# Kernel tuning notes

Hardware: AMD Instinct MI355X
Metric: run time of the kernel (lower is better)

Reference implementation:

```python
import jax, jax.numpy as jnp
import numpy as np

EPS = 1e-8
NUM_ITER = 3
NUM_SLOTS = 8
NUM_HEADS = 4


def _ln(x, w, b):
    m = x.mean(-1, keepdims=True)
    v = x.var(-1, keepdims=True)
    return (x - m) / jnp.sqrt(v + 1e-5) * w + b


def setup_inputs() -> dict:
    key = jax.random.key(0)
    B, T, N, D, S, H = 16, 12, 1024, 256, 128, 256
    K = NUM_SLOTS
    ks = jax.random.split(key, 32)
    w = lambda i, shape: (0.02 * jax.random.normal(ks[i], shape)).astype(jnp.float32)
    f32 = jnp.float32
    return {
        'inputs': jax.random.normal(ks[0], (B, T, N, D), f32),
        'slots_noise': jax.random.normal(ks[1], (B, K, S), f32),
        'slot_mu': w(2, (1, 1, S)),
        'slot_log_sigma': w(3, (1, 1, S)),
        'ln_in_w': jnp.ones((D,), f32), 'ln_in_b': jnp.zeros((D,), f32),
        'ln_slots_w': jnp.ones((S,), f32), 'ln_slots_b': jnp.zeros((S,), f32),
        'ln_mlp_w': jnp.ones((S,), f32), 'ln_mlp_b': jnp.zeros((S,), f32),
        'Wq': w(4, (S, S)), 'Wk': w(5, (D, S)), 'Wv': w(6, (D, S)),
        'gru_Wih': w(7, (3 * S, S)), 'gru_Whh': w(8, (3 * S, S)),
        'gru_bih': jnp.zeros((3 * S,), f32), 'gru_bhh': jnp.zeros((3 * S,), f32),
        'mlp_W1': w(9, (S, H)), 'mlp_b1': jnp.zeros((H,), f32),
        'mlp_W2': w(10, (H, S)), 'mlp_b2': jnp.zeros((S,), f32),
        'p_ln1_w': jnp.ones((S,), f32), 'p_ln1_b': jnp.zeros((S,), f32),
        'p_Wq': w(11, (S, S)), 'p_Wk': w(12, (S, S)), 'p_Wv': w(13, (S, S)), 'p_Wo': w(14, (S, S)),
        'p_ln2_w': jnp.ones((S,), f32), 'p_ln2_b': jnp.zeros((S,), f32),
        'p_ffn_W1': w(15, (S, 4 * S)), 'p_ffn_b1': jnp.zeros((4 * S,), f32),
        'p_ffn_W2': w(16, (4 * S, S)), 'p_ffn_b2': jnp.zeros((S,), f32),
        'p_lnf_w': jnp.ones((S,), f32), 'p_lnf_b': jnp.zeros((S,), f32),
    }


def reference(inputs, slots_noise, slot_mu, slot_log_sigma,
              ln_in_w, ln_in_b, ln_slots_w, ln_slots_b, ln_mlp_w, ln_mlp_b,
              Wq, Wk, Wv, gru_Wih, gru_Whh, gru_bih, gru_bhh,
              mlp_W1, mlp_b1, mlp_W2, mlp_b2,
              p_ln1_w, p_ln1_b, p_Wq, p_Wk, p_Wv, p_Wo,
              p_ln2_w, p_ln2_b, p_ffn_W1, p_ffn_b1, p_ffn_W2, p_ffn_b2,
              p_lnf_w, p_lnf_b):
    B, T, N, D = inputs.shape
    S = slot_mu.shape[-1]
    K = NUM_SLOTS

    slots0 = slot_mu + jnp.exp(slot_log_sigma) * slots_noise  # (B,K,S)
    x = _ln(inputs, ln_in_w, ln_in_b)
    k = (x @ Wk) * (S ** -0.5)  # (B,T,N,S), pre-scaled keys
    v = x @ Wv                  # (B,T,N,S)

    def gru(u, h):  # torch GRUCell semantics; u,h: (B*K,S)
        gi = u @ gru_Wih.T + gru_bih
        gh = h @ gru_Whh.T + gru_bhh
        i_r, i_z, i_n = jnp.split(gi, 3, -1)
        h_r, h_z, h_n = jnp.split(gh, 3, -1)
        r = jax.nn.sigmoid(i_r + h_r)
        z = jax.nn.sigmoid(i_z + h_z)
        n = jnp.tanh(i_n + r * h_n)
        return (1.0 - z) * n + z * h

    def mha(y):  # (B,K,S) self-attention, pre-LN block style
        dh = S // NUM_HEADS
        split = lambda t: t.reshape(B, K, NUM_HEADS, dh).transpose(0, 2, 1, 3)
        q = split(y @ p_Wq) * (dh ** -0.5)
        kk = split(y @ p_Wk)
        vv = split(y @ p_Wv)
        a = jax.nn.softmax(jnp.einsum('bhqd,bhkd->bhqk', q, kk), -1)
        o = jnp.einsum('bhqk,bhkd->bhqd', a, vv).transpose(0, 2, 1, 3).reshape(B, K, S)
        return o @ p_Wo

    def predictor(s):
        s = s + mha(_ln(s, p_ln1_w, p_ln1_b))
        h = _ln(s, p_ln2_w, p_ln2_b)
        s = s + (jax.nn.relu(h @ p_ffn_W1 + p_ffn_b1) @ p_ffn_W2 + p_ffn_b2)
        return _ln(s, p_lnf_w, p_lnf_b)

    def step(slots, kv_t):
        k_t, v_t = kv_t  # (B,N,S) each
        attn_vis = None
        for i in range(NUM_ITER):
            slots_prev = slots
            q = _ln(slots, ln_slots_w, ln_slots_b) @ Wq          # (B,K,S)
            logits = jnp.einsum('bns,bks->bnk', k_t, q)           # (B,N,K)
            attn_vis = jax.nn.softmax(logits, -1)                 # over slots
            attn = attn_vis + EPS
            attn = attn / attn.sum(1, keepdims=True)              # normalize over inputs
            updates = jnp.einsum('bnk,bns->bks', attn, v_t)       # (B,K,S)
            slots = gru(updates.reshape(-1, S), slots_prev.reshape(-1, S)).reshape(B, K, S)
            if i < NUM_ITER - 1:
                h = _ln(slots, ln_mlp_w, ln_mlp_b)
                slots = slots + (jax.nn.relu(h @ mlp_W1 + mlp_b1) @ mlp_W2 + mlp_b2)
        return predictor(slots), (slots, attn_vis)

    kT = jnp.swapaxes(k, 0, 1)  # (T,B,N,S)
    vT = jnp.swapaxes(v, 0, 1)
    _, (slots_seq, attn_seq) = jax.lax.scan(step, slots0, (kT, vT))
    slots_collect = jnp.swapaxes(slots_seq, 0, 1)  # (B,T,K,S)
    attns_collect = jnp.swapaxes(attn_seq, 0, 1)   # (B,T,N,K)
    return slots_collect, attns_collect
```

## Files before the change

### kernel.cpp

```cpp
#include <hip/hip_runtime.h>
#include <hip/hip_bf16.h>

typedef _Float16 half8 __attribute__((ext_vector_type(8)));
typedef float floatx4 __attribute__((ext_vector_type(4)));

#define MFMA_F16(a, b, c) __builtin_amdgcn_mfma_f32_16x16x32_f16((a), (b), (c), 0, 0, 0)

struct PrepJobs {
  const float* src[11];
  _Float16* dst[11];
  int In[11], Out[11], elems[11], doT[11];
  float scale[11];
};

__global__ void prep_all_kernel(PrepJobs J) {
  int j = blockIdx.y;
  int idx = blockIdx.x * 256 + threadIdx.x;
  if (idx >= J.elems[j]) return;
  float v;
  if (J.doT[j]) { int o = idx / J.In[j], i = idx - o * J.In[j]; v = J.src[j][i * J.Out[j] + o]; }
  else          { v = J.src[j][idx]; }
  J.dst[j][idx] = (_Float16)(v * J.scale[j]);
}

__global__ void prep_wtilde_kernel(const float* __restrict__ Wk, const float* __restrict__ Wq,
                                   _Float16* __restrict__ WT, float scale) {
  int idx = blockIdx.x * 256 + threadIdx.x;
  int s = idx >> 8, i = idx & 255;
  const float* wk = Wk + (size_t)i * 128;
  const float* wq = Wq + (size_t)s * 128;
  float acc = 0.f;
  #pragma unroll 4
  for (int o = 0; o < 128; o++) acc += wk[o] * wq[o];
  WT[idx] = (_Float16)(acc * scale);
}

__global__ void init_ctr_kernel(int* __restrict__ ctr) {
  ctr[threadIdx.x] = 0;
}

__global__ __launch_bounds__(256) void gemm_kv_kernel(
    const float* __restrict__ x, const float* __restrict__ lnw_g,
    const float* __restrict__ lnb_g, const _Float16* __restrict__ WT,
    _Float16* __restrict__ kout, _Float16* __restrict__ vTout) {
  __shared__ union {
    struct { _Float16 A[128][72]; _Float16 B[128][72]; } s;
    _Float16 C[128][136];
  } u;
  __shared__ float s_mean[128], s_rstd[128], s_red[256][2], s_lnw[256], s_lnb[256];

  const int tid = threadIdx.x;
  const int bx = blockIdx.x, y = blockIdx.y;
  const size_t r0 = (size_t)bx * 128;
  const int w = tid >> 6, lane = tid & 63, quad = lane >> 4, l15 = lane & 15;

  s_lnw[tid] = lnw_g[tid];
  s_lnb[tid] = lnb_g[tid];
  {
    int row = tid >> 1, half = tid & 1;
    const float* p = x + (r0 + row) * 256 + half * 128;
    float s = 0.f, sq = 0.f;
    for (int i = 0; i < 32; i++) {
      float4 d = ((const float4*)p)[i];
      s += d.x + d.y + d.z + d.w;
      sq += d.x * d.x + d.y * d.y + d.z * d.z + d.w * d.w;
    }
    s_red[tid][0] = s; s_red[tid][1] = sq;
  }
  __syncthreads();
  if (tid < 128) {
    float s  = s_red[2 * tid][0] + s_red[2 * tid + 1][0];
    float sq = s_red[2 * tid][1] + s_red[2 * tid + 1][1];
    float m = s * (1.f / 256.f);
    float v = sq * (1.f / 256.f) - m * m;
    s_mean[tid] = m; s_rstd[tid] = rsqrtf(v + 1e-5f);
  }

  floatx4 acc[2][8];
  for (int rt = 0; rt < 2; rt++)
    for (int ct = 0; ct < 8; ct++) acc[rt][ct] = (floatx4){0.f, 0.f, 0.f, 0.f};

  for (int c = 0; c < 4; c++) {
    __syncthreads();
    for (int i = 0; i < 4; i++) {
      int g = tid + 256 * i;
      int row = g >> 3, c8 = g & 7;
      int col0 = c * 64 + c8 * 8;
      const float* p = x + (r0 + row) * 256 + col0;
      float4 d0 = ((const float4*)p)[0];
      float4 d1 = ((const float4*)p)[1];
      float f[8] = {d0.x, d0.y, d0.z, d0.w, d1.x, d1.y, d1.z, d1.w};
      float m = s_mean[row], rs = s_rstd[row];
      half8 hv;
      #pragma unroll
      for (int j = 0; j < 8; j++)
        hv[j] = (_Float16)((f[j] - m) * rs * s_lnw[col0 + j] + s_lnb[col0 + j]);
      *(half8*)&u.s.A[row][c8 * 8] = hv;
      *(half8*)&u.s.B[row][c8 * 8] = *(const half8*)(WT + (size_t)(y * 128 + row) * 256 + col0);
    }
    __syncthreads();
    #pragma unroll
    for (int ks = 0; ks < 2; ks++) {
      half8 af[2];
      af[0] = *(const half8*)&u.s.A[(2 * w) * 16 + l15][ks * 32 + quad * 8];
      af[1] = *(const half8*)&u.s.A[(2 * w + 1) * 16 + l15][ks * 32 + quad * 8];
      #pragma unroll
      for (int ct = 0; ct < 8; ct++) {
        half8 bf = *(const half8*)&u.s.B[ct * 16 + l15][ks * 32 + quad * 8];
        acc[0][ct] = MFMA_F16(af[0], bf, acc[0][ct]);
        acc[1][ct] = MFMA_F16(af[1], bf, acc[1][ct]);
      }
    }
  }

  const size_t bt = (size_t)(bx >> 3);
  const int n0loc = (bx & 7) * 128;
  if (y == 0) {
    for (int rt = 0; rt < 2; rt++)
      for (int ct = 0; ct < 8; ct++)
        #pragma unroll
        for (int r = 0; r < 4; r++) {
          size_t row = r0 + (2 * w + rt) * 16 + quad * 4 + r;
          kout[row * 128 + ct * 16 + l15] = (_Float16)acc[rt][ct][r];
        }
  } else {
    __syncthreads();
    for (int rt = 0; rt < 2; rt++)
      for (int ct = 0; ct < 8; ct++)
        #pragma unroll
        for (int r = 0; r < 4; r++)
          u.C[(2 * w + rt) * 16 + quad * 4 + r][ct * 16 + l15] = (_Float16)acc[rt][ct][r];
    __syncthreads();
    int s = tid >> 1, hf = tid & 1;
    for (int j = 0; j < 8; j++) {
      int nb = hf * 64 + j * 8;
      half8 tmp;
      #pragma unroll
      for (int e = 0; e < 8; e++) tmp[e] = u.C[nb + e][s];
      *(half8*)(vTout + (bt * 128 + s) * 1024 + n0loc + nb) = tmp;
    }
  }
}

struct P2Args {
  const _Float16 *kbuf, *vT;
  const _Float16 *Wih, *Whh, *W1T, *W2T;
  const _Float16 *pQT, *pKT, *pVT, *pOT, *pF1T, *pF2T;
  const float *noise, *mu, *lsig;
  const float *lnsw, *lnsb, *lnmw, *lnmb;
  const float *bih, *bhh, *mb1, *mb2;
  const float *pl1w, *pl1b, *pl2w, *pl2b, *fb1, *fb2, *plfw, *plfb;
  float *out_slots, *out_attn;
  float *upd_p;
  float *col_p;
  float *vs_p;
  int   *ctr;
};

struct SH {
  _Float16 k_lds[128][136];
  _Float16 v_lds[128][136];
  float slots[8][128];
  _Float16 a16[16][136];
  _Float16 h16[16][136];
  float gi[8][384];
  float gh[8][384];
  union {
    struct { _Float16 qT[16][136]; _Float16 attnT[16][136]; } sa;
    struct { _Float16 m16[16][264]; } mlp;
    struct { float qh[8][128]; float kh[8][128]; float vh[8][128]; float sc[4][8][8]; } mha;
    struct { _Float16 f16[16][520]; } ffn;
  } u;
  float colsum[8];
  float vsum[128];
  float bih[384], bhh[384], mb1[256], mb2[128], fb1[512], fb2[128];
  float lnsw[128], lnsb[128], lnmw[128], lnmb[128];
  float pl1w[128], pl1b[128], pl2w[128], pl2b[128], plfw[128], plfb[128];
};

__device__ __forceinline__ void group_barrier(int* ctr, int target) {
  __syncthreads();
  if (threadIdx.x == 0) {
    __hip_atomic_fetch_add(ctr, 1, __ATOMIC_ACQ_REL, __HIP_MEMORY_SCOPE_AGENT);
    while (__hip_atomic_load(ctr, __ATOMIC_ACQUIRE, __HIP_MEMORY_SCOPE_AGENT) < target)
      __builtin_amdgcn_s_sleep(1);
  }
  __syncthreads();
}

__device__ __forceinline__ void ln_to_a16(SH* sh, const float (*src)[128],
                                          const float* wv, const float* bv,
                                          int w, int lane) {
  if (w < 8) {
    float x0 = src[w][lane], x1 = src[w][lane + 64];
    float s = x0 + x1, sq = x0 * x0 + x1 * x1;
    #pragma unroll
    for (int m = 1; m < 64; m <<= 1) { s += __shfl_xor(s, m); sq += __shfl_xor(sq, m); }
    float mn = s * 0.0078125f;
    float vr = sq * 0.0078125f - mn * mn;
    float rs = rsqrtf(vr + 1e-5f);
    sh->a16[w][lane]      = (_Float16)((x0 - mn) * rs * wv[lane]      + bv[lane]);
    sh->a16[w][lane + 64] = (_Float16)((x1 - mn) * rs * wv[lane + 64] + bv[lane + 64]);
  } else {
    sh->a16[w][lane] = (_Float16)0.f;
    sh->a16[w][lane + 64] = (_Float16)0.f;
  }
}

__global__ __launch_bounds__(1024, 4) void slot_attn_kernel(P2Args P) {
  __shared__ SH sh;
  const int tid = threadIdx.x;
  const int w = tid >> 6, lane = tid & 63, quad = lane >> 4, l15 = lane & 15;
  const int b = blockIdx.x & 15;
  const int g = blockIdx.x >> 4;
  const int n0 = g * 128;
  int* ctrb = P.ctr + b * 64;
  int bar_phase = 0;

  for (int i = tid; i < 384; i += 1024) { sh.bih[i] = P.bih[i]; sh.bhh[i] = P.bhh[i]; }
  for (int i = tid; i < 256; i += 1024) sh.mb1[i] = P.mb1[i];
  for (int i = tid; i < 512; i += 1024) sh.fb1[i] = P.fb1[i];
  if (tid < 128) {
    sh.mb2[tid]  = P.mb2[tid];  sh.fb2[tid]  = P.fb2[tid];
    sh.lnsw[tid] = P.lnsw[tid]; sh.lnsb[tid] = P.lnsb[tid];
    sh.lnmw[tid] = P.lnmw[tid]; sh.lnmb[tid] = P.lnmb[tid];
    sh.pl1w[tid] = P.pl1w[tid]; sh.pl1b[tid] = P.pl1b[tid];
    sh.pl2w[tid] = P.pl2w[tid]; sh.pl2b[tid] = P.pl2b[tid];
    sh.plfw[tid] = P.plfw[tid]; sh.plfb[tid] = P.plfb[tid];
  }
  {
    int kk = tid >> 7, s = tid & 127;
    sh.slots[kk][s] = P.mu[s] + expf(P.lsig[s]) * P.noise[(b * 8 + kk) * 128 + s];
  }
  __syncthreads();

  for (int t = 0; t < 12; t++) {
    const _Float16* kt = P.kbuf + ((size_t)(b * 12 + t)) * 1024 * 128 + (size_t)n0 * 128;
    const _Float16* vt = P.vT   + ((size_t)(b * 12 + t)) * 128 * 1024 + n0;
    {
      int r = tid >> 4, c8 = (tid & 15) * 8;
      #pragma unroll
      for (int p = 0; p < 2; p++) {
        int row = p * 64 + r;
        *(half8*)&sh.k_lds[row][c8] = *(const half8*)(kt + (size_t)row * 128 + c8);
        *(half8*)&sh.v_lds[row][c8] = *(const half8*)(vt + (size_t)row * 1024 + c8);
      }
    }
    if (tid < 128) sh.vsum[tid] = 0.f;
    __syncthreads();
    {
      int s = tid >> 3, j = tid & 7;
      float a = 0.f;
      #pragma unroll
      for (int e = 0; e < 16; e++) a += (float)sh.v_lds[s][j * 16 + e];
      atomicAdd(&sh.vsum[s], a);
    }
    __syncthreads();
    if (tid < 128)
      __hip_atomic_store(&P.vs_p[(b * 8 + g) * 128 + tid], sh.vsum[tid],
                         __ATOMIC_RELAXED, __HIP_MEMORY_SCOPE_AGENT);

    for (int it = 0; it < 3; it++) {
      const int par = (t * 3 + it) & 1;
      float* updg = P.upd_p + ((size_t)(par * 16 + b) * 8 + g) * 1024;
      float* colg = P.col_p + ((size_t)(par * 16 + b) * 8 + g) * 64;
      if (w < 8) {
        float x0 = sh.slots[w][lane], x1 = sh.slots[w][lane + 64];
        sh.h16[w][lane] = (_Float16)x0; sh.h16[w][lane + 64] = (_Float16)x1;
        float s = x0 + x1, sq = x0 * x0 + x1 * x1;
        #pragma unroll
        for (int m = 1; m < 64; m <<= 1) { s += __shfl_xor(s, m); sq += __shfl_xor(sq, m); }
        float mn = s * 0.0078125f;
        float vr = sq * 0.0078125f - mn * mn;
        float rs = rsqrtf(vr + 1e-5f);
        sh.a16[w][lane]      = (_Float16)((x0 - mn) * rs * sh.lnsw[lane]      + sh.lnsb[lane]);
        sh.a16[w][lane + 64] = (_Float16)((x1 - mn) * rs * sh.lnsw[lane + 64] + sh.lnsb[lane + 64]);
      } else {
        sh.h16[w][lane] = (_Float16)0.f; sh.h16[w][lane + 64] = (_Float16)0.f;
        sh.a16[w][lane] = (_Float16)0.f; sh.a16[w][lane + 64] = (_Float16)0.f;
      }
      if (tid < 8) sh.colsum[tid] = 0.f;
      __syncthreads();
      if (w < 8) {
        int nloc0 = w * 16;
        floatx4 acc = (floatx4){0.f, 0.f, 0.f, 0.f};
        const _Float16* ar = &sh.k_lds[nloc0 + l15][quad * 8];
        const _Float16* br = &sh.a16[l15][quad * 8];
        #pragma unroll
        for (int ks = 0; ks < 4; ks++)
          acc = MFMA_F16(*(const half8*)(ar + ks * 32), *(const half8*)(br + ks * 32), acc);
        float cs = 0.f;
        #pragma unroll
        for (int r = 0; r < 4; r++) {
          float v = (l15 < 8) ? acc[r] : -3.0e38f;
          float mx = v;
          mx = fmaxf(mx, __shfl_xor(mx, 1, 16));
          mx = fmaxf(mx, __shfl_xor(mx, 2, 16));
          mx = fmaxf(mx, __shfl_xor(mx, 4, 16));
          mx = fmaxf(mx, __shfl_xor(mx, 8, 16));
          float pv = (l15 < 8) ? expf(v - mx) : 0.f;
          float ss = pv;
          ss += __shfl_xor(ss, 1, 16); ss += __shfl_xor(ss, 2, 16);
          ss += __shfl_xor(ss, 4, 16); ss += __shfl_xor(ss, 8, 16);
          float pn = pv / ss;
          cs += pn;
          int nloc = nloc0 + quad * 4 + r;
          sh.u.sa.attnT[l15][nloc] = (_Float16)pn;
          if (it == 2 && l15 < 8)
            P.out_attn[((size_t)(b * 12 + t) * 1024 + n0 + nloc) * 8 + l15] = pn;
        }
        cs += __shfl_xor(cs, 16); cs += __shfl_xor(cs, 32);
        if (lane < 8) atomicAdd(&sh.colsum[lane], cs);
      } else {
        const int idx8 = w - 8;
        const _Float16* ar = &sh.h16[l15][quad * 8];
        #pragma unroll
        for (int tt = 0; tt < 2; tt++) {
          int ct = idx8 + tt * 8;
          const _Float16* Bg = P.Whh + (size_t)(ct * 16 + l15) * 128 + quad * 8;
          floatx4 acc = (floatx4){0.f, 0.f, 0.f, 0.f};
          #pragma unroll
          for (int ks = 0; ks < 4; ks++)
            acc = MFMA_F16(*(const half8*)(ar + ks * 32), *(const half8*)(Bg + ks * 32), acc);
          int col = ct * 16 + l15;
          #pragma unroll
          for (int r = 0; r < 4; r++) {
            int slot = quad * 4 + r;
            if (slot < 8) sh.gh[slot][col] = acc[r] + sh.bhh[col];
          }
        }
      }
      __syncthreads();
      if (w < 8) {
        floatx4 acc = (floatx4){0.f, 0.f, 0.f, 0.f};
        const _Float16* ar = &sh.u.sa.attnT[l15][quad * 8];
        const _Float16* br = &sh.v_lds[w * 16 + l15][quad * 8];
        #pragma unroll
        for (int ks = 0; ks < 4; ks++)
          acc = MFMA_F16(*(const half8*)(ar + ks * 32), *(const half8*)(br + ks * 32), acc);
        int scol = w * 16 + l15;
        #pragma unroll
        for (int r = 0; r < 4; r++) {
          int slot = quad * 4 + r;
          if (slot < 8)
            __hip_atomic_store(&updg[slot * 128 + scol], acc[r],
                               __ATOMIC_RELAXED, __HIP_MEMORY_SCOPE_AGENT);
        }
      } else {
        const int idx8 = w - 8;
        int ct = idx8 + 16;
        const _Float16* ar = &sh.h16[l15][quad * 8];
        const _Float16* Bg = P.Whh + (size_t)(ct * 16 + l15) * 128 + quad * 8;
        floatx4 acc = (floatx4){0.f, 0.f, 0.f, 0.f};
        #pragma unroll
        for (int ks = 0; ks < 4; ks++)
          acc = MFMA_F16(*(const half8*)(ar + ks * 32), *(const half8*)(Bg + ks * 32), acc);
        int col = ct * 16 + l15;
        #pragma unroll
        for (int r = 0; r < 4; r++) {
          int slot = quad * 4 + r;
          if (slot < 8) sh.gh[slot][col] = acc[r] + sh.bhh[col];
        }
      }
      if (tid < 8)
        __hip_atomic_store(&colg[tid], sh.colsum[tid],
                           __ATOMIC_RELAXED, __HIP_MEMORY_SCOPE_AGENT);
      bar_phase++;
      group_barrier(ctrb, 8 * bar_phase);
      {
        int slot = tid >> 7, scol = tid & 127;
        const float* up = P.upd_p + (size_t)(par * 16 + b) * 8 * 1024 + slot * 128 + scol;
        float sum = 0.f;
        #pragma unroll
        for (int gg = 0; gg < 8; gg++)
          sum += __hip_atomic_load((float*)(up + gg * 1024),
                                   __ATOMIC_RELAXED, __HIP_MEMORY_SCOPE_AGENT);
        const float* cp = P.col_p + (size_t)(par * 16 + b) * 8 * 64 + slot;
        float csum = 0.f;
        #pragma unroll
        for (int gg = 0; gg < 8; gg++)
          csum += __hip_atomic_load((float*)(cp + gg * 64),
                                    __ATOMIC_RELAXED, __HIP_MEMORY_SCOPE_AGENT);
        float vsv;
        if (it == 0) {
          const float* vp = P.vs_p + b * 8 * 128 + scol;
          float vtot = 0.f;
          #pragma unroll
          for (int gg = 0; gg < 8; gg++)
            vtot += __hip_atomic_load((float*)(vp + gg * 128),
                                      __ATOMIC_RELAXED, __HIP_MEMORY_SCOPE_AGENT);
          if (slot == 0) sh.vsum[scol] = vtot;
          vsv = vtot;
        } else {
          vsv = sh.vsum[scol];
        }
        float upd = (sum + 1e-8f * vsv) / (csum + 1024.f * 1e-8f);
        sh.a16[slot][scol] = (_Float16)upd;
      }
      __syncthreads();
      {
        const _Float16* ar = &sh.a16[l15][quad * 8];
        const _Float16* Bg = P.Wih + (size_t)(w * 16 + l15) * 128 + quad * 8;
        floatx4 acc = (floatx4){0.f, 0.f, 0.f, 0.f};
        #pragma unroll
        for (int ks = 0; ks < 4; ks++)
          acc = MFMA_F16(*(const half8*)(ar + ks * 32), *(const half8*)(Bg + ks * 32), acc);
        int col = w * 16 + l15;
        #pragma unroll
        for (int r = 0; r < 4; r++) {
          int slot = quad * 4 + r;
          if (slot < 8) sh.gi[slot][col] = acc[r] + sh.bih[col];
        }
        if (w < 8) {
          int col2 = (16 + w) * 16 + l15;
          const _Float16* Bg2 = P.Wih + (size_t)((16 + w) * 16 + l15) * 128 + quad * 8;
          floatx4 acc2 = (floatx4){0.f, 0.f, 0.f, 0.f};
          #pragma unroll
          for (int ks = 0; ks < 4; ks++)
            acc2 = MFMA_F16(*(const half8*)(ar + ks * 32), *(const half8*)(Bg2 + ks * 32), acc2);
          #pragma unroll
          for (int r = 0; r < 4; r++) {
            int slot = quad * 4 + r;
            if (slot < 8) sh.gi[slot][col2] = acc2[r] + sh.bih[col2];
          }
        }
      }
      __syncthreads();
      if (w < 8) {
        float h0 = sh.slots[w][lane], h1 = sh.slots[w][lane + 64];
        float r0 = 1.f / (1.f + expf(-(sh.gi[w][lane]       + sh.gh[w][lane])));
        float z0 = 1.f / (1.f + expf(-(sh.gi[w][128 + lane] + sh.gh[w][128 + lane])));
        float n0v = tanhf(sh.gi[w][256 + lane] + r0 * sh.gh[w][256 + lane]);
        float x0 = (1.f - z0) * n0v + z0 * h0;
        int l64 = lane + 64;
        float r1 = 1.f / (1.f + expf(-(sh.gi[w][l64]       + sh.gh[w][l64])));
        float z1 = 1.f / (1.f + expf(-(sh.gi[w][128 + l64] + sh.gh[w][128 + l64])));
        float n1v = tanhf(sh.gi[w][256 + l64] + r1 * sh.gh[w][256 + l64]);
        float x1 = (1.f - z1) * n1v + z1 * h1;
        sh.slots[w][lane] = x0; sh.slots[w][lane + 64] = x1;
        if (it == 2 && g == 0) {
          P.out_slots[((size_t)(b * 12 + t) * 8 + w) * 128 + lane]      = x0;
          P.out_slots[((size_t)(b * 12 + t) * 8 + w) * 128 + lane + 64] = x1;
        }
        const float* wv = (it < 2) ? sh.lnmw : sh.pl1w;
        const float* bv = (it < 2) ? sh.lnmb : sh.pl1b;
        float s = x0 + x1, sq = x0 * x0 + x1 * x1;
        #pragma unroll
        for (int m = 1; m < 64; m <<= 1) { s += __shfl_xor(s, m); sq += __shfl_xor(sq, m); }
        float mn = s * 0.0078125f;
        float vr = sq * 0.0078125f - mn * mn;
        float rs = rsqrtf(vr + 1e-5f);
        sh.a16[w][lane]      = (_Float16)((x0 - mn) * rs * wv[lane]      + bv[lane]);
        sh.a16[w][lane + 64] = (_Float16)((x1 - mn) * rs * wv[lane + 64] + bv[lane + 64]);
      }
      __syncthreads();
      if (it < 2) {
        {
          floatx4 acc = (floatx4){0.f, 0.f, 0.f, 0.f};
          const _Float16* ar = &sh.a16[l15][quad * 8];
          const _Float16* br = P.W1T + (size_t)(w * 16 + l15) * 128 + quad * 8;
          #pragma unroll
          for (int ks = 0; ks < 4; ks++)
            acc = MFMA_F16(*(const half8*)(ar + ks * 32), *(const half8*)(br + ks * 32), acc);
          int col = w * 16 + l15;
          #pragma unroll
          for (int r = 0; r < 4; r++) {
            int slot = quad * 4 + r;
            if (slot < 8) sh.u.mlp.m16[slot][col] = (_Float16)fmaxf(acc[r] + sh.mb1[col], 0.f);
            else          sh.u.mlp.m16[slot][col] = (_Float16)0.f;
          }
        }
        __syncthreads();
        if (w < 8) {
          floatx4 acc = (floatx4){0.f, 0.f, 0.f, 0.f};
          const _Float16* ar = &sh.u.mlp.m16[l15][quad * 8];
          const _Float16* br = P.W2T + (size_t)(w * 16 + l15) * 256 + quad * 8;
          #pragma unroll
          for (int ks = 0; ks < 8; ks++)
            acc = MFMA_F16(*(const half8*)(ar + ks * 32), *(const half8*)(br + ks * 32), acc);
          int col = w * 16 + l15;
          #pragma unroll
          for (int r = 0; r < 4; r++) {
            int slot = quad * 4 + r;
            if (slot < 8) sh.slots[slot][col] += acc[r] + sh.mb2[col];
          }
        }
        __syncthreads();
      }
    }

    {
      const _Float16* ar = &sh.a16[l15][quad * 8];
      int gg = w >> 3, ct = w & 7, col = ct * 16 + l15;
      const _Float16* Bg = (gg == 0 ? P.pQT : P.pKT) + (size_t)(ct * 16 + l15) * 128 + quad * 8;
      floatx4 acc = (floatx4){0.f, 0.f, 0.f, 0.f};
      #pragma unroll
      for (int ks = 0; ks < 4; ks++)
        acc = MFMA_F16(*(const half8*)(ar + ks * 32), *(const half8*)(Bg + ks * 32), acc);
      float scale = (gg == 0) ? 0.17677669529663687f : 1.f;
      float* dst = (gg == 0) ? &sh.u.mha.qh[0][0] : &sh.u.mha.kh[0][0];
      #pragma unroll
      for (int r = 0; r < 4; r++) {
        int slot = quad * 4 + r;
        if (slot < 8) dst[slot * 128 + col] = acc[r] * scale;
      }
      if (w < 8) {
        const _Float16* Bg2 = P.pVT + (size_t)(w * 16 + l15) * 128 + quad * 8;
        floatx4 a2 = (floatx4){0.f, 0.f, 0.f, 0.f};
        #pragma unroll
        for (int ks = 0; ks < 4; ks++)
          a2 = MFMA_F16(*(const half8*)(ar + ks * 32), *(const half8*)(Bg2 + ks * 32), a2);
        int colv = w * 16 + l15;
        #pragma unroll
        for (int r = 0; r < 4; r++) {
          int slot = quad * 4 + r;
          if (slot < 8) sh.u.mha.vh[slot][colv] = a2[r];
        }
      }
    }
    __syncthreads();
    if (w < 4) {
      int h = w, a = lane >> 3, b2 = lane & 7;
      const float* qr = &sh.u.mha.qh[a][h * 32];
      const float* kr = &sh.u.mha.kh[b2][h * 32];
      float s = 0.f;
      #pragma unroll
      for (int d = 0; d < 32; d++) s += qr[d] * kr[d];
      float mx = s;
      mx = fmaxf(mx, __shfl_xor(mx, 1, 8));
      mx = fmaxf(mx, __shfl_xor(mx, 2, 8));
      mx = fmaxf(mx, __shfl_xor(mx, 4, 8));
      float e = expf(s - mx);
      float ssum = e;
      ssum += __shfl_xor(ssum, 1, 8); ssum += __shfl_xor(ssum, 2, 8); ssum += __shfl_xor(ssum, 4, 8);
      float p = e / ssum;
      float o0 = 0.f, o1 = 0.f, o2 = 0.f, o3 = 0.f;
      int d0 = h * 32 + b2 * 4;
      #pragma unroll
      for (int j = 0; j < 8; j++) {
        float pj = __shfl(p, (a << 3) + j);
        const float* vr = &sh.u.mha.vh[j][d0];
        o0 += pj * vr[0]; o1 += pj * vr[1]; o2 += pj * vr[2]; o3 += pj * vr[3];
      }
      sh.a16[a][d0]     = (_Float16)o0;
      sh.a16[a][d0 + 1] = (_Float16)o1;
      sh.a16[a][d0 + 2] = (_Float16)o2;
      sh.a16[a][d0 + 3] = (_Float16)o3;
    }
    __syncthreads();
    if (w < 8) {
      floatx4 acc = (floatx4){0.f, 0.f, 0.f, 0.f};
      const _Float16* ar = &sh.a16[l15][quad * 8];
      const _Float16* br = P.pOT + (size_t)(w * 16 + l15) * 128 + quad * 8;
      #pragma unroll
      for (int ks = 0; ks < 4; ks++)
        acc = MFMA_F16(*(const half8*)(ar + ks * 32), *(const half8*)(br + ks * 32), acc);
      int col = w * 16 + l15;
      #pragma unroll
      for (int r = 0; r < 4; r++) {
        int slot = quad * 4 + r;
        if (slot < 8) sh.slots[slot][col] += acc[r];
      }
    }
    __syncthreads();
    ln_to_a16(&sh, sh.slots, sh.pl2w, sh.pl2b, w, lane);
    __syncthreads();
    for (int ct = w; ct < 32; ct += 16) {
      floatx4 acc = (floatx4){0.f, 0.f, 0.f, 0.f};
      const _Float16* ar = &sh.a16[l15][quad * 8];
      const _Float16* br = P.pF1T + (size_t)(ct * 16 + l15) * 128 + quad * 8;
      #pragma unroll
      for (int ks = 0; ks < 4; ks++)
        acc = MFMA_F16(*(const half8*)(ar + ks * 32), *(const half8*)(br + ks * 32), acc);
      int col = ct * 16 + l15;
      #pragma unroll
      for (int r = 0; r < 4; r++) {
        int slot = quad * 4 + r;
        if (slot < 8) sh.u.ffn.f16[slot][col] = (_Float16)fmaxf(acc[r] + sh.fb1[col], 0.f);
        else          sh.u.ffn.f16[slot][col] = (_Float16)0.f;
      }
    }
    __syncthreads();
    if (w < 8) {
      floatx4 acc = (floatx4){0.f, 0.f, 0.f, 0.f};
      const _Float16* ar = &sh.u.ffn.f16[l15][quad * 8];
      const _Float16* br = P.pF2T + (size_t)(w * 16 + l15) * 512 + quad * 8;
      #pragma unroll 4
      for (int ks = 0; ks < 16; ks++)
        acc = MFMA_F16(*(const half8*)(ar + ks * 32), *(const half8*)(br + ks * 32), acc);
      int col = w * 16 + l15;
      #pragma unroll
      for (int r = 0; r < 4; r++) {
        int slot = quad * 4 + r;
        if (slot < 8) sh.slots[slot][col] += acc[r] + sh.fb2[col];
      }
    }
    __syncthreads();
    if (w < 8) {
      float x0 = sh.slots[w][lane], x1 = sh.slots[w][lane + 64];
      float s = x0 + x1, sq = x0 * x0 + x1 * x1;
      #pragma unroll
      for (int m = 1; m < 64; m <<= 1) { s += __shfl_xor(s, m); sq += __shfl_xor(sq, m); }
      float mn = s * 0.0078125f;
      float vr = sq * 0.0078125f - mn * mn;
      float rs = rsqrtf(vr + 1e-5f);
      sh.slots[w][lane]      = (x0 - mn) * rs * sh.plfw[lane]      + sh.plfb[lane];
      sh.slots[w][lane + 64] = (x1 - mn) * rs * sh.plfw[lane + 64] + sh.plfb[lane + 64];
    }
    __syncthreads();
  }
}

extern "C" void kernel_launch(void* const* d_in, const int* in_sizes, int n_in,
                              void* d_out, int out_size, void* d_ws, size_t ws_size,
                              hipStream_t stream) {
  const float* inp   = (const float*)d_in[0];
  const float* noise = (const float*)d_in[1];
  const float* mu    = (const float*)d_in[2];
  const float* lsig  = (const float*)d_in[3];
  const float* lniw  = (const float*)d_in[4];
  const float* lnib  = (const float*)d_in[5];
  const float* lnsw  = (const float*)d_in[6];
  const float* lnsb  = (const float*)d_in[7];
  const float* lnmw  = (const float*)d_in[8];
  const float* lnmb  = (const float*)d_in[9];
  const float* Wq    = (const float*)d_in[10];
  const float* Wk    = (const float*)d_in[11];
  const float* Wv    = (const float*)d_in[12];
  const float* gWih  = (const float*)d_in[13];
  const float* gWhh  = (const float*)d_in[14];
  const float* gbih  = (const float*)d_in[15];
  const float* gbhh  = (const float*)d_in[16];
  const float* mW1   = (const float*)d_in[17];
  const float* mb1   = (const float*)d_in[18];
  const float* mW2   = (const float*)d_in[19];
  const float* mb2   = (const float*)d_in[20];
  const float* pl1w  = (const float*)d_in[21];
  const float* pl1b  = (const float*)d_in[22];
  const float* pWq   = (const float*)d_in[23];
  const float* pWk   = (const float*)d_in[24];
  const float* pWv   = (const float*)d_in[25];
  const float* pWo   = (const float*)d_in[26];
  const float* pl2w  = (const float*)d_in[27];
  const float* pl2b  = (const float*)d_in[28];
  const float* pf1   = (const float*)d_in[29];
  const float* pfb1  = (const float*)d_in[30];
  const float* pf2   = (const float*)d_in[31];
  const float* pfb2  = (const float*)d_in[32];
  const float* plfw  = (const float*)d_in[33];
  const float* plfb  = (const float*)d_in[34];

  _Float16* p   = (_Float16*)d_ws;
  _Float16* kbuf = p;  p += 25165824;
  _Float16* vT   = p;  p += 25165824;
  _Float16* WT   = p;  p += 65536;
  _Float16* WqT  = p;  p += 16384;
  _Float16* Wih  = p;  p += 49152;
  _Float16* Whh  = p;  p += 49152;
  _Float16* W1T  = p;  p += 32768;
  _Float16* W2T  = p;  p += 32768;
  _Float16* pQT  = p;  p += 16384;
  _Float16* pKT  = p;  p += 16384;
  _Float16* pVT  = p;  p += 16384;
  _Float16* pOT  = p;  p += 16384;
  _Float16* pF1T = p;  p += 65536;
  _Float16* pF2T = p;  p += 65536;
  float* fb   = (float*)p;
  float* upd_p = fb;  fb += 2 * 16 * 8 * 1024;
  float* col_p = fb;  fb += 2 * 16 * 8 * 64;
  float* vs_p  = fb;  fb += 16 * 8 * 128;
  int*   ctr   = (int*)fb;
  (void)WqT;

  const float kscale = 0.08838834764831845f;
  init_ctr_kernel<<<1, 1024, 0, stream>>>(ctr);

  PrepJobs J;
  const float* srcs[11] = {Wv, gWih, gWhh, mW1, mW2, pWq, pWk, pWv, pWo, pf1, pf2};
  _Float16* dsts[11]    = {WT + 32768, Wih, Whh, W1T, W2T, pQT, pKT, pVT, pOT, pF1T, pF2T};
  int Ins[11]    = {256, 49152, 49152, 128, 256, 128, 128, 128, 128, 128, 512};
  int Outs[11]   = {128, 1, 1, 256, 128, 128, 128, 128, 128, 512, 128};
  int elemss[11] = {32768, 49152, 49152, 32768, 32768, 16384, 16384, 16384, 16384, 65536, 65536};
  int doTs[11]   = {1, 0, 0, 1, 1, 1, 1, 1, 1, 1, 1};
  float scales[11] = {1.f, 1.f, 1.f, 1.f, 1.f, 1.f, 1.f, 1.f, 1.f, 1.f, 1.f};
  for (int j = 0; j < 11; j++) {
    J.src[j] = srcs[j]; J.dst[j] = dsts[j]; J.In[j] = Ins[j]; J.Out[j] = Outs[j];
    J.elems[j] = elemss[j]; J.doT[j] = doTs[j]; J.scale[j] = scales[j];
  }
  dim3 gp(256, 11, 1);
  prep_all_kernel<<<gp, 256, 0, stream>>>(J);
  prep_wtilde_kernel<<<128, 256, 0, stream>>>(Wk, Wq, WT, kscale);

  dim3 g1(1536, 2, 1);
  gemm_kv_kernel<<<g1, 256, 0, stream>>>(inp, lniw, lnib, WT, kbuf, vT);

  P2Args a;
  a.kbuf = kbuf; a.vT = vT;
  a.Wih = Wih; a.Whh = Whh; a.W1T = W1T; a.W2T = W2T;
  a.pQT = pQT; a.pKT = pKT; a.pVT = pVT; a.pOT = pOT; a.pF1T = pF1T; a.pF2T = pF2T;
  a.noise = noise; a.mu = mu; a.lsig = lsig;
  a.lnsw = lnsw; a.lnsb = lnsb; a.lnmw = lnmw; a.lnmb = lnmb;
  a.bih = gbih; a.bhh = gbhh; a.mb1 = mb1; a.mb2 = mb2;
  a.pl1w = pl1w; a.pl1b = pl1b; a.pl2w = pl2w; a.pl2b = pl2b;
  a.fb1 = pfb1; a.fb2 = pfb2; a.plfw = plfw; a.plfb = plfb;
  a.out_slots = (float*)d_out;
  a.out_attn  = (float*)d_out + 196608;
  a.upd_p = upd_p; a.col_p = col_p; a.vs_p = vs_p; a.ctr = ctr;

  slot_attn_kernel<<<128, 1024, 0, stream>>>(a);
}
```

Measured before the change: 1.244 ms.

## Run one workgroup per batch in slot attention, dropping cross-block barriers

The recurrent slot-attention kernel now uses one 1024-thread workgroup per batch element (16 blocks) instead of 8 cooperating blocks per batch, which synchronised through global atomics and a spin barrier. Keys and values are read directly from global memory for all 1024 inputs. The value column sum is obtained by adding a row of ones to the attention matrix inside the MFMA. Partial updates and column sums are reduced in LDS instead of global scratch. This removes the inter-block barrier latency and global atomic traffic, but only 16 CUs do the work and each block streams all of its K/V per iteration without LDS staging.

```diff
diff --git a/kernel.cpp b/kernel.cpp
--- a/kernel.cpp
+++ b/kernel.cpp
@@ -35,10 +35,6 @@
   WT[idx] = (_Float16)(acc * scale);
 }
 
-__global__ void init_ctr_kernel(int* __restrict__ ctr) {
-  ctr[threadIdx.x] = 0;
-}
-
 __global__ __launch_bounds__(256) void gemm_kv_kernel(
     const float* __restrict__ x, const float* __restrict__ lnw_g,
     const float* __restrict__ lnb_g, const _Float16* __restrict__ WT,
@@ -151,42 +147,24 @@
   const float *bih, *bhh, *mb1, *mb2;
   const float *pl1w, *pl1b, *pl2w, *pl2b, *fb1, *fb2, *plfw, *plfb;
   float *out_slots, *out_attn;
-  float *upd_p;
-  float *col_p;
-  float *vs_p;
-  int   *ctr;
 };
 
 struct SH {
-  _Float16 k_lds[128][136];
-  _Float16 v_lds[128][136];
   float slots[8][128];
   _Float16 a16[16][136];
   _Float16 h16[16][136];
   float gi[8][384];
   float gh[8][384];
   union {
-    struct { _Float16 qT[16][136]; _Float16 attnT[16][136]; } sa;
+    struct { _Float16 attnT[16][1032]; float updh[2][9][128]; float wcs[16][8]; } sa;
     struct { _Float16 m16[16][264]; } mlp;
     struct { float qh[8][128]; float kh[8][128]; float vh[8][128]; float sc[4][8][8]; } mha;
     struct { _Float16 f16[16][520]; } ffn;
   } u;
-  float colsum[8];
-  float vsum[128];
   float bih[384], bhh[384], mb1[256], mb2[128], fb1[512], fb2[128];
   float lnsw[128], lnsb[128], lnmw[128], lnmb[128];
   float pl1w[128], pl1b[128], pl2w[128], pl2b[128], plfw[128], plfb[128];
 };
-
-__device__ __forceinline__ void group_barrier(int* ctr, int target) {
-  __syncthreads();
-  if (threadIdx.x == 0) {
-    __hip_atomic_fetch_add(ctr, 1, __ATOMIC_ACQ_REL, __HIP_MEMORY_SCOPE_AGENT);
-    while (__hip_atomic_load(ctr, __ATOMIC_ACQUIRE, __HIP_MEMORY_SCOPE_AGENT) < target)
-      __builtin_amdgcn_s_sleep(1);
-  }
-  __syncthreads();
-}
 
 __device__ __forceinline__ void ln_to_a16(SH* sh, const float (*src)[128],
                                           const float* wv, const float* bv,
@@ -211,11 +189,7 @@
   __shared__ SH sh;
   const int tid = threadIdx.x;
   const int w = tid >> 6, lane = tid & 63, quad = lane >> 4, l15 = lane & 15;
-  const int b = blockIdx.x & 15;
-  const int g = blockIdx.x >> 4;
-  const int n0 = g * 128;
-  int* ctrb = P.ctr + b * 64;
-  int bar_phase = 0;
+  const int b = blockIdx.x;
 
   for (int i = tid; i < 384; i += 1024) { sh.bih[i] = P.bih[i]; sh.bhh[i] = P.bhh[i]; }
   for (int i = tid; i < 256; i += 1024) sh.mb1[i] = P.mb1[i];
@@ -230,43 +204,23 @@
   }
   {
     int kk = tid >> 7, s = tid & 127;
-    sh.slots[kk][s] = P.mu[s] + expf(P.lsig[s]) * P.noise[(b * 8 + kk) * 128 + s];
+    float v = P.mu[s] + expf(P.lsig[s]) * P.noise[(b * 8 + kk) * 128 + s];
+    sh.slots[kk][s] = v;
+    sh.h16[kk][s] = (_Float16)v;
+  }
+  if (w >= 8) {
+    sh.a16[w][lane] = (_Float16)0.f; sh.a16[w][lane + 64] = (_Float16)0.f;
+    sh.h16[w][lane] = (_Float16)0.f; sh.h16[w][lane + 64] = (_Float16)0.f;
   }
   __syncthreads();
 
   for (int t = 0; t < 12; t++) {
-    const _Float16* kt = P.kbuf + ((size_t)(b * 12 + t)) * 1024 * 128 + (size_t)n0 * 128;
-    const _Float16* vt = P.vT   + ((size_t)(b * 12 + t)) * 128 * 1024 + n0;
-    {
-      int r = tid >> 4, c8 = (tid & 15) * 8;
-      #pragma unroll
-      for (int p = 0; p < 2; p++) {
-        int row = p * 64 + r;
-        *(half8*)&sh.k_lds[row][c8] = *(const half8*)(kt + (size_t)row * 128 + c8);
-        *(half8*)&sh.v_lds[row][c8] = *(const half8*)(vt + (size_t)row * 1024 + c8);
-      }
-    }
-    if (tid < 128) sh.vsum[tid] = 0.f;
-    __syncthreads();
-    {
-      int s = tid >> 3, j = tid & 7;
-      float a = 0.f;
-      #pragma unroll
-      for (int e = 0; e < 16; e++) a += (float)sh.v_lds[s][j * 16 + e];
-      atomicAdd(&sh.vsum[s], a);
-    }
-    __syncthreads();
-    if (tid < 128)
-      __hip_atomic_store(&P.vs_p[(b * 8 + g) * 128 + tid], sh.vsum[tid],
-                         __ATOMIC_RELAXED, __HIP_MEMORY_SCOPE_AGENT);
+    const _Float16* kt = P.kbuf + ((size_t)(b * 12 + t)) * 1024 * 128;
+    const _Float16* vt = P.vT   + ((size_t)(b * 12 + t)) * 128 * 1024;
 
     for (int it = 0; it < 3; it++) {
-      const int par = (t * 3 + it) & 1;
-      float* updg = P.upd_p + ((size_t)(par * 16 + b) * 8 + g) * 1024;
-      float* colg = P.col_p + ((size_t)(par * 16 + b) * 8 + g) * 64;
       if (w < 8) {
         float x0 = sh.slots[w][lane], x1 = sh.slots[w][lane + 64];
-        sh.h16[w][lane] = (_Float16)x0; sh.h16[w][lane + 64] = (_Float16)x1;
         float s = x0 + x1, sq = x0 * x0 + x1 * x1;
         #pragma unroll
         for (int m = 1; m < 64; m <<= 1) { s += __shfl_xor(s, m); sq += __shfl_xor(sq, m); }
@@ -276,46 +230,10 @@
         sh.a16[w][lane]      = (_Float16)((x0 - mn) * rs * sh.lnsw[lane]      + sh.lnsb[lane]);
         sh.a16[w][lane + 64] = (_Float16)((x1 - mn) * rs * sh.lnsw[lane + 64] + sh.lnsb[lane + 64]);
       } else {
-        sh.h16[w][lane] = (_Float16)0.f; sh.h16[w][lane + 64] = (_Float16)0.f;
-        sh.a16[w][lane] = (_Float16)0.f; sh.a16[w][lane + 64] = (_Float16)0.f;
-      }
-      if (tid < 8) sh.colsum[tid] = 0.f;
-      __syncthreads();
-      if (w < 8) {
-        int nloc0 = w * 16;
-        floatx4 acc = (floatx4){0.f, 0.f, 0.f, 0.f};
-        const _Float16* ar = &sh.k_lds[nloc0 + l15][quad * 8];
-        const _Float16* br = &sh.a16[l15][quad * 8];
-        #pragma unroll
-        for (int ks = 0; ks < 4; ks++)
-          acc = MFMA_F16(*(const half8*)(ar + ks * 32), *(const half8*)(br + ks * 32), acc);
-        float cs = 0.f;
-        #pragma unroll
-        for (int r = 0; r < 4; r++) {
-          float v = (l15 < 8) ? acc[r] : -3.0e38f;
-          float mx = v;
-          mx = fmaxf(mx, __shfl_xor(mx, 1, 16));
-          mx = fmaxf(mx, __shfl_xor(mx, 2, 16));
-          mx = fmaxf(mx, __shfl_xor(mx, 4, 16));
-          mx = fmaxf(mx, __shfl_xor(mx, 8, 16));
-          float pv = (l15 < 8) ? expf(v - mx) : 0.f;
-          float ss = pv;
-          ss += __shfl_xor(ss, 1, 16); ss += __shfl_xor(ss, 2, 16);
-          ss += __shfl_xor(ss, 4, 16); ss += __shfl_xor(ss, 8, 16);
-          float pn = pv / ss;
-          cs += pn;
-          int nloc = nloc0 + quad * 4 + r;
-          sh.u.sa.attnT[l15][nloc] = (_Float16)pn;
-          if (it == 2 && l15 < 8)
-            P.out_attn[((size_t)(b * 12 + t) * 1024 + n0 + nloc) * 8 + l15] = pn;
-        }
-        cs += __shfl_xor(cs, 16); cs += __shfl_xor(cs, 32);
-        if (lane < 8) atomicAdd(&sh.colsum[lane], cs);
-      } else {
         const int idx8 = w - 8;
         const _Float16* ar = &sh.h16[l15][quad * 8];
         #pragma unroll
-        for (int tt = 0; tt < 2; tt++) {
+        for (int tt = 0; tt < 3; tt++) {
           int ct = idx8 + tt * 8;
           const _Float16* Bg = P.Whh + (size_t)(ct * 16 + l15) * 128 + quad * 8;
           floatx4 acc = (floatx4){0.f, 0.f, 0.f, 0.f};
@@ -331,70 +249,71 @@
         }
       }
       __syncthreads();
-      if (w < 8) {
+      {
+        floatx4 accs[4];
+        #pragma unroll
+        for (int tt = 0; tt < 4; tt++) {
+          int nbase = (w + tt * 16) * 16;
+          floatx4 acc = (floatx4){0.f, 0.f, 0.f, 0.f};
+          const _Float16* ar = kt + (size_t)(nbase + l15) * 128 + quad * 8;
+          const _Float16* br = &sh.a16[l15][quad * 8];
+          #pragma unroll
+          for (int ks = 0; ks < 4; ks++)
+            acc = MFMA_F16(*(const half8*)(ar + ks * 32), *(const half8*)(br + ks * 32), acc);
+          accs[tt] = acc;
+        }
+        float cs = 0.f;
+        #pragma unroll
+        for (int tt = 0; tt < 4; tt++) {
+          int nbase = (w + tt * 16) * 16;
+          #pragma unroll
+          for (int r = 0; r < 4; r++) {
+            float v = (l15 < 8) ? accs[tt][r] : -3.0e38f;
+            float mx = v;
+            mx = fmaxf(mx, __shfl_xor(mx, 1, 16));
+            mx = fmaxf(mx, __shfl_xor(mx, 2, 16));
+            mx = fmaxf(mx, __shfl_xor(mx, 4, 16));
+            mx = fmaxf(mx, __shfl_xor(mx, 8, 16));
+            float pv = (l15 < 8) ? expf(v - mx) : 0.f;
+            float ss = pv;
+            ss += __shfl_xor(ss, 1, 16); ss += __shfl_xor(ss, 2, 16);
+            ss += __shfl_xor(ss, 4, 16); ss += __shfl_xor(ss, 8, 16);
+            float pn = pv / ss;
+            cs += pn;
+            int n = nbase + quad * 4 + r;
+            sh.u.sa.attnT[l15][n] = (l15 == 8) ? (_Float16)1.f : (_Float16)pn;
+            if (it == 2 && l15 < 8)
+              P.out_attn[((size_t)(b * 12 + t) * 1024 + n) * 8 + l15] = pn;
+          }
+        }
+        cs += __shfl_xor(cs, 16); cs += __shfl_xor(cs, 32);
+        if (lane < 8) sh.u.sa.wcs[w][lane] = cs;
+      }
+      __syncthreads();
+      {
+        int tcol = w & 7, h = w >> 3;
         floatx4 acc = (floatx4){0.f, 0.f, 0.f, 0.f};
-        const _Float16* ar = &sh.u.sa.attnT[l15][quad * 8];
-        const _Float16* br = &sh.v_lds[w * 16 + l15][quad * 8];
-        #pragma unroll
-        for (int ks = 0; ks < 4; ks++)
+        const _Float16* ar = &sh.u.sa.attnT[l15][h * 512 + quad * 8];
+        const _Float16* br = vt + (size_t)(tcol * 16 + l15) * 1024 + h * 512 + quad * 8;
+        #pragma unroll 4
+        for (int ks = 0; ks < 16; ks++)
           acc = MFMA_F16(*(const half8*)(ar + ks * 32), *(const half8*)(br + ks * 32), acc);
-        int scol = w * 16 + l15;
+        int scol = tcol * 16 + l15;
         #pragma unroll
         for (int r = 0; r < 4; r++) {
-          int slot = quad * 4 + r;
-          if (slot < 8)
-            __hip_atomic_store(&updg[slot * 128 + scol], acc[r],
-                               __ATOMIC_RELAXED, __HIP_MEMORY_SCOPE_AGENT);
-        }
-      } else {
-        const int idx8 = w - 8;
-        int ct = idx8 + 16;
-        const _Float16* ar = &sh.h16[l15][quad * 8];
-        const _Float16* Bg = P.Whh + (size_t)(ct * 16 + l15) * 128 + quad * 8;
-        floatx4 acc = (floatx4){0.f, 0.f, 0.f, 0.f};
-        #pragma unroll
-        for (int ks = 0; ks < 4; ks++)
-          acc = MFMA_F16(*(const half8*)(ar + ks * 32), *(const half8*)(Bg + ks * 32), acc);
-        int col = ct * 16 + l15;
-        #pragma unroll
-        for (int r = 0; r < 4; r++) {
-          int slot = quad * 4 + r;
-          if (slot < 8) sh.gh[slot][col] = acc[r] + sh.bhh[col];
-        }
-      }
-      if (tid < 8)
-        __hip_atomic_store(&colg[tid], sh.colsum[tid],
-                           __ATOMIC_RELAXED, __HIP_MEMORY_SCOPE_AGENT);
-      bar_phase++;
-      group_barrier(ctrb, 8 * bar_phase);
+          int row = quad * 4 + r;
+          if (row < 9) sh.u.sa.updh[h][row][scol] = acc[r];
+        }
+      }
+      __syncthreads();
       {
         int slot = tid >> 7, scol = tid & 127;
-        const float* up = P.upd_p + (size_t)(par * 16 + b) * 8 * 1024 + slot * 128 + scol;
-        float sum = 0.f;
-        #pragma unroll
-        for (int gg = 0; gg < 8; gg++)
-          sum += __hip_atomic_load((float*)(up + gg * 1024),
-                                   __ATOMIC_RELAXED, __HIP_MEMORY_SCOPE_AGENT);
-        const float* cp = P.col_p + (size_t)(par * 16 + b) * 8 * 64 + slot;
+        float sum = sh.u.sa.updh[0][slot][scol] + sh.u.sa.updh[1][slot][scol];
+        float vs  = sh.u.sa.updh[0][8][scol]    + sh.u.sa.updh[1][8][scol];
         float csum = 0.f;
         #pragma unroll
-        for (int gg = 0; gg < 8; gg++)
-          csum += __hip_atomic_load((float*)(cp + gg * 64),
-                                    __ATOMIC_RELAXED, __HIP_MEMORY_SCOPE_AGENT);
-        float vsv;
-        if (it == 0) {
-          const float* vp = P.vs_p + b * 8 * 128 + scol;
-          float vtot = 0.f;
-          #pragma unroll
-          for (int gg = 0; gg < 8; gg++)
-            vtot += __hip_atomic_load((float*)(vp + gg * 128),
-                                      __ATOMIC_RELAXED, __HIP_MEMORY_SCOPE_AGENT);
-          if (slot == 0) sh.vsum[scol] = vtot;
-          vsv = vtot;
-        } else {
-          vsv = sh.vsum[scol];
-        }
-        float upd = (sum + 1e-8f * vsv) / (csum + 1024.f * 1e-8f);
+        for (int ww = 0; ww < 16; ww++) csum += sh.u.sa.wcs[ww][slot];
+        float upd = (sum + 1e-8f * vs) / (csum + 1024.f * 1e-8f);
         sh.a16[slot][scol] = (_Float16)upd;
       }
       __syncthreads();
@@ -438,7 +357,7 @@
         float n1v = tanhf(sh.gi[w][256 + l64] + r1 * sh.gh[w][256 + l64]);
         float x1 = (1.f - z1) * n1v + z1 * h1;
         sh.slots[w][lane] = x0; sh.slots[w][lane + 64] = x1;
-        if (it == 2 && g == 0) {
+        if (it == 2) {
           P.out_slots[((size_t)(b * 12 + t) * 8 + w) * 128 + lane]      = x0;
           P.out_slots[((size_t)(b * 12 + t) * 8 + w) * 128 + lane + 64] = x1;
         }
@@ -482,7 +401,11 @@
           #pragma unroll
           for (int r = 0; r < 4; r++) {
             int slot = quad * 4 + r;
-            if (slot < 8) sh.slots[slot][col] += acc[r] + sh.mb2[col];
+            if (slot < 8) {
+              float ns = sh.slots[slot][col] + acc[r] + sh.mb2[col];
+              sh.slots[slot][col] = ns;
+              sh.h16[slot][col] = (_Float16)ns;
+            }
           }
         }
         __syncthreads();
@@ -604,8 +527,10 @@
       float mn = s * 0.0078125f;
       float vr = sq * 0.0078125f - mn * mn;
       float rs = rsqrtf(vr + 1e-5f);
-      sh.slots[w][lane]      = (x0 - mn) * rs * sh.plfw[lane]      + sh.plfb[lane];
-      sh.slots[w][lane + 64] = (x1 - mn) * rs * sh.plfw[lane + 64] + sh.plfb[lane + 64];
+      float y0 = (x0 - mn) * rs * sh.plfw[lane]      + sh.plfb[lane];
+      float y1 = (x1 - mn) * rs * sh.plfw[lane + 64] + sh.plfb[lane + 64];
+      sh.slots[w][lane] = y0;      sh.slots[w][lane + 64] = y1;
+      sh.h16[w][lane] = (_Float16)y0; sh.h16[w][lane + 64] = (_Float16)y1;
     }
     __syncthreads();
   }
@@ -665,15 +590,9 @@
   _Float16* pOT  = p;  p += 16384;
   _Float16* pF1T = p;  p += 65536;
   _Float16* pF2T = p;  p += 65536;
-  float* fb   = (float*)p;
-  float* upd_p = fb;  fb += 2 * 16 * 8 * 1024;
-  float* col_p = fb;  fb += 2 * 16 * 8 * 64;
-  float* vs_p  = fb;  fb += 16 * 8 * 128;
-  int*   ctr   = (int*)fb;
   (void)WqT;
 
   const float kscale = 0.08838834764831845f;
-  init_ctr_kernel<<<1, 1024, 0, stream>>>(ctr);
 
   PrepJobs J;
   const float* srcs[11] = {Wv, gWih, gWhh, mW1, mW2, pWq, pWk, pWv, pWo, pf1, pf2};
@@ -705,7 +624,6 @@
   a.fb1 = pfb1; a.fb2 = pfb2; a.plfw = plfw; a.plfb = plfb;
   a.out_slots = (float*)d_out;
   a.out_attn  = (float*)d_out + 196608;
-  a.upd_p = upd_p; a.col_p = col_p; a.vs_p = vs_p; a.ctr = ctr;
-
-  slot_attn_kernel<<<128, 1024, 0, stream>>>(a);
+
+  slot_attn_kernel<<<16, 1024, 0, stream>>>(a);
 }
```

Result: slower. 1.916 ms (+54.1%).

## Compute both K and V outputs in one GEMM block to reuse LayerNormed input

Applied to the files above, without the earlier changes.

The K/V projection GEMM previously launched two blocks per row tile (y=0 for K, y=1 for V), each re-reading the fp32 input and recomputing its LayerNorm. Now each block loads the normalized input tile once and multiplies it against both weight halves, keeping two accumulator sets. Input traffic and LN work are halved. In exchange the block uses twice the accumulator registers and more LDS, which may reduce occupancy. An unused qT buffer and the WqT workspace slot are also removed.

```diff
diff --git a/kernel.cpp b/kernel.cpp
--- a/kernel.cpp
+++ b/kernel.cpp
@@ -44,13 +44,13 @@
     const float* __restrict__ lnb_g, const _Float16* __restrict__ WT,
     _Float16* __restrict__ kout, _Float16* __restrict__ vTout) {
   __shared__ union {
-    struct { _Float16 A[128][72]; _Float16 B[128][72]; } s;
+    struct { _Float16 A[128][72]; _Float16 B0[128][72]; _Float16 B1[128][72]; } s;
     _Float16 C[128][136];
   } u;
   __shared__ float s_mean[128], s_rstd[128], s_red[256][2], s_lnw[256], s_lnb[256];
 
   const int tid = threadIdx.x;
-  const int bx = blockIdx.x, y = blockIdx.y;
+  const int bx = blockIdx.x;
   const size_t r0 = (size_t)bx * 128;
   const int w = tid >> 6, lane = tid & 63, quad = lane >> 4, l15 = lane & 15;
 
@@ -76,9 +76,12 @@
     s_mean[tid] = m; s_rstd[tid] = rsqrtf(v + 1e-5f);
   }
 
-  floatx4 acc[2][8];
+  floatx4 acc0[2][8], acc1[2][8];
   for (int rt = 0; rt < 2; rt++)
-    for (int ct = 0; ct < 8; ct++) acc[rt][ct] = (floatx4){0.f, 0.f, 0.f, 0.f};
+    for (int ct = 0; ct < 8; ct++) {
+      acc0[rt][ct] = (floatx4){0.f, 0.f, 0.f, 0.f};
+      acc1[rt][ct] = (floatx4){0.f, 0.f, 0.f, 0.f};
+    }
 
   for (int c = 0; c < 4; c++) {
     __syncthreads();
@@ -96,41 +99,43 @@
       for (int j = 0; j < 8; j++)
         hv[j] = (_Float16)((f[j] - m) * rs * s_lnw[col0 + j] + s_lnb[col0 + j]);
       *(half8*)&u.s.A[row][c8 * 8] = hv;
-      *(half8*)&u.s.B[row][c8 * 8] = *(const half8*)(WT + (size_t)(y * 128 + row) * 256 + col0);
+      *(half8*)&u.s.B0[row][c8 * 8] = *(const half8*)(WT + (size_t)row * 256 + col0);
+      *(half8*)&u.s.B1[row][c8 * 8] = *(const half8*)(WT + (size_t)(128 + row) * 256 + col0);
     }
     __syncthreads();
     #pragma unroll
     for (int ks = 0; ks < 2; ks++) {
-      half8 af[2];
-      af[0] = *(const half8*)&u.s.A[(2 * w) * 16 + l15][ks * 32 + quad * 8];
-      af[1] = *(const half8*)&u.s.A[(2 * w + 1) * 16 + l15][ks * 32 + quad * 8];
+      half8 af0 = *(const half8*)&u.s.A[(2 * w) * 16 + l15][ks * 32 + quad * 8];
+      half8 af1 = *(const half8*)&u.s.A[(2 * w + 1) * 16 + l15][ks * 32 + quad * 8];
       #pragma unroll
       for (int ct = 0; ct < 8; ct++) {
-        half8 bf = *(const half8*)&u.s.B[ct * 16 + l15][ks * 32 + quad * 8];
-        acc[0][ct] = MFMA_F16(af[0], bf, acc[0][ct]);
-        acc[1][ct] = MFMA_F16(af[1], bf, acc[1][ct]);
+        half8 b0 = *(const half8*)&u.s.B0[ct * 16 + l15][ks * 32 + quad * 8];
+        acc0[0][ct] = MFMA_F16(af0, b0, acc0[0][ct]);
+        acc0[1][ct] = MFMA_F16(af1, b0, acc0[1][ct]);
+        half8 b1 = *(const half8*)&u.s.B1[ct * 16 + l15][ks * 32 + quad * 8];
+        acc1[0][ct] = MFMA_F16(af0, b1, acc1[0][ct]);
+        acc1[1][ct] = MFMA_F16(af1, b1, acc1[1][ct]);
       }
     }
   }
 
   const size_t bt = (size_t)(bx >> 3);
   const int n0loc = (bx & 7) * 128;
-  if (y == 0) {
-    for (int rt = 0; rt < 2; rt++)
-      for (int ct = 0; ct < 8; ct++)
-        #pragma unroll
-        for (int r = 0; r < 4; r++) {
-          size_t row = r0 + (2 * w + rt) * 16 + quad * 4 + r;
-          kout[row * 128 + ct * 16 + l15] = (_Float16)acc[rt][ct][r];
-        }
-  } else {
-    __syncthreads();
-    for (int rt = 0; rt < 2; rt++)
-      for (int ct = 0; ct < 8; ct++)
-        #pragma unroll
-        for (int r = 0; r < 4; r++)
-          u.C[(2 * w + rt) * 16 + quad * 4 + r][ct * 16 + l15] = (_Float16)acc[rt][ct][r];
-    __syncthreads();
+  for (int rt = 0; rt < 2; rt++)
+    for (int ct = 0; ct < 8; ct++)
+      #pragma unroll
+      for (int r = 0; r < 4; r++) {
+        size_t row = r0 + (2 * w + rt) * 16 + quad * 4 + r;
+        kout[row * 128 + ct * 16 + l15] = (_Float16)acc0[rt][ct][r];
+      }
+  __syncthreads();
+  for (int rt = 0; rt < 2; rt++)
+    for (int ct = 0; ct < 8; ct++)
+      #pragma unroll
+      for (int r = 0; r < 4; r++)
+        u.C[(2 * w + rt) * 16 + quad * 4 + r][ct * 16 + l15] = (_Float16)acc1[rt][ct][r];
+  __syncthreads();
+  {
     int s = tid >> 1, hf = tid & 1;
     for (int j = 0; j < 8; j++) {
       int nb = hf * 64 + j * 8;
@@ -166,7 +171,7 @@
   float gi[8][384];
   float gh[8][384];
   union {
-    struct { _Float16 qT[16][136]; _Float16 attnT[16][136]; } sa;
+    struct { _Float16 attnT[16][136]; } sa;
     struct { _Float16 m16[16][264]; } mlp;
     struct { float qh[8][128]; float kh[8][128]; float vh[8][128]; float sc[4][8][8]; } mha;
     struct { _Float16 f16[16][520]; } ffn;
@@ -654,7 +659,6 @@
   _Float16* kbuf = p;  p += 25165824;
   _Float16* vT   = p;  p += 25165824;
   _Float16* WT   = p;  p += 65536;
-  _Float16* WqT  = p;  p += 16384;
   _Float16* Wih  = p;  p += 49152;
   _Float16* Whh  = p;  p += 49152;
   _Float16* W1T  = p;  p += 32768;
@@ -670,7 +674,6 @@
   float* col_p = fb;  fb += 2 * 16 * 8 * 64;
   float* vs_p  = fb;  fb += 16 * 8 * 128;
   int*   ctr   = (int*)fb;
-  (void)WqT;
 
   const float kscale = 0.08838834764831845f;
   init_ctr_kernel<<<1, 1024, 0, stream>>>(ctr);
@@ -691,8 +694,7 @@
   prep_all_kernel<<<gp, 256, 0, stream>>>(J);
   prep_wtilde_kernel<<<128, 256, 0, stream>>>(Wk, Wq, WT, kscale);
 
-  dim3 g1(1536, 2, 1);
-  gemm_kv_kernel<<<g1, 256, 0, stream>>>(inp, lniw, lnib, WT, kbuf, vT);
+  gemm_kv_kernel<<<1536, 256, 0, stream>>>(inp, lniw, lnib, WT, kbuf, vT);
 
   P2Args a;
   a.kbuf = kbuf; a.vT = vT;
```

After: 1.211 ms. 1.03x faster.
